# Kernel optimization log

Hardware: AMD Instinct MI355X
Metric: run time of the kernel (lower is better)

Reference implementation:

```python
import jax, jax.numpy as jnp
import numpy as np
import math

B, S, H = 2, 2048, 2048
NH, LD = 16, 512
HD = H // NH


def setup_inputs() -> dict:
    key = jax.random.key(0)
    ks = jax.random.split(key, 9)
    sc = 0.02
    return {
        "x": jax.random.normal(ks[0], (B, S, H), dtype=jnp.float32),
        "wq": jax.random.normal(ks[1], (H, H), dtype=jnp.float32) * sc,
        "bq": jnp.zeros((H,), dtype=jnp.float32),
        "wk_lat": jax.random.normal(ks[2], (H, LD), dtype=jnp.float32) * sc,
        "wv_lat": jax.random.normal(ks[3], (H, LD), dtype=jnp.float32) * sc,
        "wk": jax.random.normal(ks[4], (LD, H), dtype=jnp.float32) * sc,
        "wv": jax.random.normal(ks[5], (LD, H), dtype=jnp.float32) * sc,
        "wo": jax.random.normal(ks[6], (H, H), dtype=jnp.float32) * sc,
        "bo": jnp.zeros((H,), dtype=jnp.float32),
    }


def reference(x, wq, bq, wk_lat, wv_lat, wk, wv, wo, bo):
    b, s, _ = x.shape
    # projections
    q = (x @ wq + bq).reshape(b, s, NH, HD).transpose(0, 2, 1, 3)  # [B,NH,S,HD]
    k_lat = x @ wk_lat  # [B,S,LD]
    v_lat = x @ wv_lat
    k = (k_lat @ wk).reshape(b, s, NH, HD).transpose(0, 2, 1, 3)
    v = (v_lat @ wv).reshape(b, s, NH, HD).transpose(0, 2, 1, 3)
    # causal attention
    scores = jnp.einsum('bhqd,bhkd->bhqk', q, k) / math.sqrt(HD)
    mask = jnp.tril(jnp.ones((s, s), dtype=bool))  # True = keep
    scores = jnp.where(mask, scores, -jnp.inf)
    weights = jax.nn.softmax(scores, axis=-1)
    out = jnp.einsum('bhqk,bhkd->bhqd', weights, v)
    out = out.transpose(0, 2, 1, 3).reshape(b, s, H)
    return out @ wo + bo
```

## Files before the change

### kernel.cpp

```cpp
#include <hip/hip_runtime.h>
#include <hip/hip_bf16.h>

#define PB   2
#define PS   2048
#define PH   2048
#define PNH  16
#define PLD  512
#define PHD  128
#define PM   (PB * PS)
#define PNCAT 3072
#define ATT_SCALE 0.08838834764831845f
#define ATT_MOFF 4.0f

typedef __attribute__((ext_vector_type(8))) short bf16x8;
typedef __attribute__((ext_vector_type(4))) float f32x4;

__device__ __forceinline__ float bf2f(unsigned int h) {
    return __uint_as_float(h << 16);
}
__device__ __forceinline__ unsigned short f2bf(float f) {
    unsigned int u = __float_as_uint(f);
    u += 0x7FFFu + ((u >> 16) & 1u);
    return (unsigned short)(u >> 16);
}

__device__ __forceinline__ void gl_lds16(const unsigned short* g, unsigned short* l) {
    __builtin_amdgcn_global_load_lds(
        (const __attribute__((address_space(1))) unsigned int*)g,
        (__attribute__((address_space(3))) unsigned int*)l, 16, 0, 0);
}

__global__ __launch_bounds__(256) void cast_f32_bf16_kernel(
    const float* __restrict__ in, unsigned short* __restrict__ out, int n)
{
    int i = (blockIdx.x * 256 + threadIdx.x) * 4;
    if (i >= n) return;
    float4 f = *(const float4*)(in + i);
    unsigned int a = (unsigned int)f2bf(f.x) | ((unsigned int)f2bf(f.y) << 16);
    unsigned int b = (unsigned int)f2bf(f.z) | ((unsigned int)f2bf(f.w) << 16);
    *(uint2*)(out + i) = make_uint2(a, b);
}

__global__ __launch_bounds__(256) void transpose_cast_kernel(
    const float* __restrict__ in, unsigned short* __restrict__ out, int R, int C)
{
    __shared__ float tile[32][33];
    int tx = threadIdx.x, ty = threadIdx.y;
    int r0 = blockIdx.y * 32, c0 = blockIdx.x * 32;
#pragma unroll
    for (int i = 0; i < 32; i += 8)
        tile[ty + i][tx] = in[(size_t)(r0 + ty + i) * C + (c0 + tx)];
    __syncthreads();
#pragma unroll
    for (int i = 0; i < 32; i += 8)
        out[(size_t)(c0 + ty + i) * R + (r0 + tx)] = f2bf(tile[tx][ty + i]);
}

template<int EPI, bool HAS_BIAS>
__global__ __launch_bounds__(256) void gemm128_kernel(
    const unsigned short* __restrict__ A, int lda,
    const unsigned short* __restrict__ BT,
    const float* __restrict__ bias, int nbias,
    void* __restrict__ Cout, int ldc,
    int M, int N, int K)
{
    __shared__ __align__(16) unsigned short As[128 * 32];
    __shared__ __align__(16) unsigned short Bs[128 * 32];

    const int tid  = threadIdx.x;
    const int wave = tid >> 6;
    const int lane = tid & 63;
    const int wm = wave >> 1, wn = wave & 1;
    const int quad = lane >> 4, l15 = lane & 15;
    const int bm = blockIdx.y * 128, bn = blockIdx.x * 128;

    f32x4 acc[4][4] = {};

    const int srow = wave * 32 + (lane >> 2);
    const int scol = (lane & 3) * 8;
    const unsigned short* aG = A  + (size_t)(bm + srow) * lda + scol;
    const unsigned short* bG = BT + (size_t)(bn + srow) * K + scol;
    unsigned short* aL = &As[wave * 32 * 32];
    unsigned short* bL = &Bs[wave * 32 * 32];

    for (int k0 = 0; k0 < K; k0 += 32) {
        gl_lds16(aG + k0,                    aL);
        gl_lds16(aG + k0 + (size_t)16 * lda, aL + 16 * 32);
        gl_lds16(bG + k0,                    bL);
        gl_lds16(bG + k0 + (size_t)16 * K,   bL + 16 * 32);
        __syncthreads();
        bf16x8 af[4], bfr[4];
#pragma unroll
        for (int i = 0; i < 4; ++i) {
            af[i]  = *(const bf16x8*)&As[(wm * 64 + i * 16 + l15) * 32 + quad * 8];
            bfr[i] = *(const bf16x8*)&Bs[(wn * 64 + i * 16 + l15) * 32 + quad * 8];
        }
#pragma unroll
        for (int i = 0; i < 4; ++i)
#pragma unroll
            for (int j = 0; j < 4; ++j)
                acc[i][j] = __builtin_amdgcn_mfma_f32_16x16x32_bf16(af[i], bfr[j], acc[i][j], 0, 0, 0);
        __syncthreads();
    }

#pragma unroll
    for (int i = 0; i < 4; ++i)
#pragma unroll
        for (int j = 0; j < 4; ++j)
#pragma unroll
            for (int r = 0; r < 4; ++r) {
                int row = bm + wm * 64 + i * 16 + quad * 4 + r;
                int col = bn + wn * 64 + j * 16 + l15;
                float val = acc[i][j][r];
                if (HAS_BIAS && col < nbias) val += bias[col];
                if (EPI == 2) {
                    int bb = row >> 11, s = row & 2047, hh = col >> 7, d = col & 127;
                    size_t idx = ((size_t)((bb << 4) + hh) << 18) + ((size_t)(s >> 6) << 13)
                               + ((d >> 3) << 9) + ((s & 63) << 3) + (d & 7);
                    ((unsigned short*)Cout)[idx] = f2bf(val);
                } else if (EPI == 3) {
                    int bb = row >> 11, s = row & 2047, hh = col >> 7, d = col & 127;
                    size_t idx = ((size_t)((bb << 4) + hh) << 18) + ((size_t)(s >> 6) << 13)
                               + (((s >> 3) & 7) << 10) + (d << 3) + (s & 7);
                    ((unsigned short*)Cout)[idx] = f2bf(val);
                } else if (EPI == 1) {
                    ((float*)Cout)[(size_t)row * ldc + col] = val;
                } else {
                    ((unsigned short*)Cout)[(size_t)row * ldc + col] = f2bf(val);
                }
            }
}

__global__ __launch_bounds__(256) void flash_attn_mfma_kernel(
    const unsigned short* __restrict__ q,
    const unsigned short* __restrict__ kswz,
    const unsigned short* __restrict__ vswz,
    unsigned short* __restrict__ o)
{
    __shared__ __align__(16) unsigned short Kl[2][8192];
    __shared__ __align__(16) unsigned short Vl[8192];
    __shared__ __align__(16) unsigned short Ps[4][16][72];

    const int tid  = threadIdx.x;
    const int wave = tid >> 6;
    const int lane = tid & 63;
    const int quad = lane >> 4, l15 = lane & 15;

    const int bid = blockIdx.x;
    const int qt = 31 - (bid >> 5);
    const int bh = bid & 31;
    const int b  = bh >> 4, h = bh & 15;
    const int q0 = qt * 64;

    const unsigned short* qbase = q + (size_t)(b * PS + q0) * PNCAT + h * PHD;
    const unsigned short* kbase = kswz + ((size_t)bh << 18);
    const unsigned short* vbase = vswz + ((size_t)bh << 18);

    auto stageK = [&](int it, int buf) {
        const unsigned short* kt = kbase + ((size_t)it << 13);
#pragma unroll
        for (int j = 0; j < 4; ++j)
            gl_lds16(kt + (wave * 4 + j) * 512 + lane * 8, &Kl[buf][(wave * 4 + j) * 512]);
    };
    auto stageV = [&](int it) {
        const unsigned short* vt = vbase + ((size_t)it << 13);
#pragma unroll
        for (int j = 0; j < 4; ++j)
            gl_lds16(vt + (wave * 4 + j) * 512 + lane * 8, &Vl[(wave * 4 + j) * 512]);
    };

    bf16x8 aq[4];
#pragma unroll
    for (int kk = 0; kk < 4; ++kk)
        aq[kk] = *(const bf16x8*)(qbase + (size_t)(wave * 16 + l15) * PNCAT + kk * 32 + quad * 8);

    bf16x8 vones;
#pragma unroll
    for (int j = 0; j < 8; ++j) vones[j] = (short)0x3F80;

    f32x4 oacc[8] = {};
    f32x4 lacc = {};

    stageK(0, 0);

    for (int it = 0; it <= qt; ++it) {
        const int cur = it & 1;
        __syncthreads();
        stageV(it);
        if (it < qt) stageK(it + 1, cur ^ 1);

        f32x4 sacc[4] = {};
#pragma unroll
        for (int kk = 0; kk < 4; ++kk)
#pragma unroll
            for (int n = 0; n < 4; ++n) {
                bf16x8 bk = *(const bf16x8*)&Kl[cur][((kk * 4 + quad) * 64 + n * 16 + l15) * 8];
                sacc[n] = __builtin_amdgcn_mfma_f32_16x16x32_bf16(aq[kk], bk, sacc[n], 0, 0, 0);
            }

        const bool diag = (it == qt);
#pragma unroll
        for (int n = 0; n < 4; ++n)
#pragma unroll
            for (int r = 0; r < 4; ++r) {
                float p = __expf(fmaf(sacc[n][r], ATT_SCALE, -ATT_MOFF));
                if (diag && (n * 16 + l15 > wave * 16 + quad * 4 + r)) p = 0.0f;
                Ps[wave][quad * 4 + r][n * 16 + l15] = f2bf(p);
            }

        __syncthreads();

#pragma unroll
        for (int kk = 0; kk < 2; ++kk) {
            bf16x8 ap = *(const bf16x8*)&Ps[wave][l15][kk * 32 + quad * 8];
            lacc = __builtin_amdgcn_mfma_f32_16x16x32_bf16(ap, vones, lacc, 0, 0, 0);
#pragma unroll
            for (int n = 0; n < 8; ++n) {
                bf16x8 bv = *(const bf16x8*)&Vl[((kk * 4 + quad) * 128 + n * 16 + l15) * 8];
                oacc[n] = __builtin_amdgcn_mfma_f32_16x16x32_bf16(ap, bv, oacc[n], 0, 0, 0);
            }
        }
    }

    float inv[4];
#pragma unroll
    for (int r = 0; r < 4; ++r) inv[r] = 1.0f / lacc[r];
#pragma unroll
    for (int n = 0; n < 8; ++n)
#pragma unroll
        for (int r = 0; r < 4; ++r) {
            int row = q0 + wave * 16 + quad * 4 + r;
            int col = h * PHD + n * 16 + l15;
            o[(size_t)(b * PS + row) * PH + col] = f2bf(oacc[n][r] * inv[r]);
        }
}

extern "C" void kernel_launch(void* const* d_in, const int* in_sizes, int n_in,
                              void* d_out, int out_size, void* d_ws, size_t ws_size,
                              hipStream_t stream)
{
    const float* x      = (const float*)d_in[0];
    const float* wq     = (const float*)d_in[1];
    const float* bq     = (const float*)d_in[2];
    const float* wk_lat = (const float*)d_in[3];
    const float* wv_lat = (const float*)d_in[4];
    const float* wk     = (const float*)d_in[5];
    const float* wv     = (const float*)d_in[6];
    const float* wo     = (const float*)d_in[7];
    const float* bo     = (const float*)d_in[8];
    float* out = (float*)d_out;

    char* ws = (char*)d_ws;
    size_t off = 0;
    auto alloc = [&](size_t bytes) -> void* {
        void* p = ws + off;
        off += (bytes + 255) & ~(size_t)255;
        return p;
    };
    unsigned short* xb    = (unsigned short*)alloc((size_t)PM * PH * 2);
    unsigned short* wcatT = (unsigned short*)alloc((size_t)PNCAT * PH * 2);
    unsigned short* wkT   = (unsigned short*)alloc((size_t)PH * PLD * 2);
    unsigned short* wvT   = (unsigned short*)alloc((size_t)PH * PLD * 2);
    unsigned short* woT   = (unsigned short*)alloc((size_t)PH * PH * 2);
    unsigned short* cat   = (unsigned short*)alloc((size_t)PM * PNCAT * 2);
    unsigned short* kswz  = (unsigned short*)alloc((size_t)PM * PH * 2);
    unsigned short* attn  = (unsigned short*)alloc((size_t)PM * PH * 2);
    unsigned short* vswz  = xb;

    unsigned short* wqT    = wcatT;
    unsigned short* wkLatT = wcatT + (size_t)PH * PH;
    unsigned short* wvLatT = wcatT + (size_t)(PH + PLD) * PH;

    dim3 tb(32, 8);

    cast_f32_bf16_kernel<<<(PM * PH) / 4 / 256, 256, 0, stream>>>(x, xb, PM * PH);
    transpose_cast_kernel<<<dim3(PH / 32,  PH / 32),  tb, 0, stream>>>(wq,     wqT,    PH,  PH);
    transpose_cast_kernel<<<dim3(PLD / 32, PH / 32),  tb, 0, stream>>>(wk_lat, wkLatT, PH,  PLD);
    transpose_cast_kernel<<<dim3(PLD / 32, PH / 32),  tb, 0, stream>>>(wv_lat, wvLatT, PH,  PLD);
    transpose_cast_kernel<<<dim3(PH / 32,  PLD / 32), tb, 0, stream>>>(wk,     wkT,    PLD, PH);
    transpose_cast_kernel<<<dim3(PH / 32,  PLD / 32), tb, 0, stream>>>(wv,     wvT,    PLD, PH);
    transpose_cast_kernel<<<dim3(PH / 32,  PH / 32),  tb, 0, stream>>>(wo,     woT,    PH,  PH);

    gemm128_kernel<0, true><<<dim3(PNCAT / 128, PM / 128), 256, 0, stream>>>(
        xb, PH, wcatT, bq, PH, cat, PNCAT, PM, PNCAT, PH);

    gemm128_kernel<2, false><<<dim3(PH / 128, PM / 128), 256, 0, stream>>>(
        cat + PH, PNCAT, wkT, nullptr, 0, kswz, 0, PM, PH, PLD);
    gemm128_kernel<3, false><<<dim3(PH / 128, PM / 128), 256, 0, stream>>>(
        cat + PH + PLD, PNCAT, wvT, nullptr, 0, vswz, 0, PM, PH, PLD);

    flash_attn_mfma_kernel<<<PB * PNH * (PS / 64), 256, 0, stream>>>(cat, kswz, vswz, attn);

    gemm128_kernel<1, true><<<dim3(PH / 128, PM / 128), 256, 0, stream>>>(
        attn, PH, woT, bo, PH, out, PH, PM, PH, PH);
}
```

Measured before the change: 381.9 us.

## Replace 128x128 GEMM with 8-wave double-buffered swizzled 256-wide pipelined GEMM

Swaps the simple single-buffered 128x128 bf16 MFMA GEMM for an 8-wave kernel with 256-wide (BM x 256) tiles, K-step 64, and double-buffered LDS filled by direct global-to-LDS loads interleaved across four compute phases. The LDS layout is XOR-swizzled to avoid bank conflicts, and workgroups are remapped across XCDs for L2 locality. s_setprio and explicit waitcnt/barriers are used to overlap loads with MFMA. The goal is to hide memory latency and raise MFMA utilization in the projection GEMMs, at the cost of more LDS per block, more registers and more complex synchronization.

```diff
diff --git a/kernel.cpp b/kernel.cpp
--- a/kernel.cpp
+++ b/kernel.cpp
@@ -15,9 +15,6 @@
 typedef __attribute__((ext_vector_type(8))) short bf16x8;
 typedef __attribute__((ext_vector_type(4))) float f32x4;
 
-__device__ __forceinline__ float bf2f(unsigned int h) {
-    return __uint_as_float(h << 16);
-}
 __device__ __forceinline__ unsigned short f2bf(float f) {
     unsigned int u = __float_as_uint(f);
     u += 0x7FFFu + ((u >> 16) & 1u);
@@ -29,6 +26,10 @@
         (const __attribute__((address_space(1))) unsigned int*)g,
         (__attribute__((address_space(3))) unsigned int*)l, 16, 0, 0);
 }
+
+#define VMCNT(n)   asm volatile("s_waitcnt vmcnt(" #n ")" ::: "memory")
+#define LGKM0()    asm volatile("s_waitcnt lgkmcnt(0)" ::: "memory")
+#define MEMFENCE() asm volatile("" ::: "memory")
 
 __global__ __launch_bounds__(256) void cast_f32_bf16_kernel(
     const float* __restrict__ in, unsigned short* __restrict__ out, int n)
@@ -56,62 +57,171 @@
         out[(size_t)(c0 + ty + i) * R + (r0 + tx)] = f2bf(tile[tx][ty + i]);
 }
 
-template<int EPI, bool HAS_BIAS>
-__global__ __launch_bounds__(256) void gemm128_kernel(
+template<int BM, int EPI, bool HAS_BIAS>
+__global__ __launch_bounds__(512, 2) void gemm8p_kernel(
     const unsigned short* __restrict__ A, int lda,
     const unsigned short* __restrict__ BT,
     const float* __restrict__ bias, int nbias,
-    void* __restrict__ Cout, int ldc,
-    int M, int N, int K)
+    void* __restrict__ Cout, int ldc, int K)
 {
-    __shared__ __align__(16) unsigned short As[128 * 32];
-    __shared__ __align__(16) unsigned short Bs[128 * 32];
+    constexpr int AH  = BM / 128;
+    constexpr int MR  = BM / 32;
+    constexpr int MH  = MR / 2;
+    constexpr int ASZ = BM * 64;
+    __shared__ __align__(16) unsigned short lds[2 * ASZ + 32768];
 
     const int tid  = threadIdx.x;
-    const int wave = tid >> 6;
-    const int lane = tid & 63;
-    const int wm = wave >> 1, wn = wave & 1;
+    const int wave = tid >> 6, lane = tid & 63;
+    const int wm = wave >> 2, wn = wave & 3;
     const int quad = lane >> 4, l15 = lane & 15;
-    const int bm = blockIdx.y * 128, bn = blockIdx.x * 128;
-
-    f32x4 acc[4][4] = {};
-
-    const int srow = wave * 32 + (lane >> 2);
-    const int scol = (lane & 3) * 8;
-    const unsigned short* aG = A  + (size_t)(bm + srow) * lda + scol;
-    const unsigned short* bG = BT + (size_t)(bn + srow) * K + scol;
-    unsigned short* aL = &As[wave * 32 * 32];
-    unsigned short* bL = &Bs[wave * 32 * 32];
-
-    for (int k0 = 0; k0 < K; k0 += 32) {
-        gl_lds16(aG + k0,                    aL);
-        gl_lds16(aG + k0 + (size_t)16 * lda, aL + 16 * 32);
-        gl_lds16(bG + k0,                    bL);
-        gl_lds16(bG + k0 + (size_t)16 * K,   bL + 16 * 32);
-        __syncthreads();
-        bf16x8 af[4], bfr[4];
-#pragma unroll
-        for (int i = 0; i < 4; ++i) {
-            af[i]  = *(const bf16x8*)&As[(wm * 64 + i * 16 + l15) * 32 + quad * 8];
-            bfr[i] = *(const bf16x8*)&Bs[(wn * 64 + i * 16 + l15) * 32 + quad * 8];
-        }
-#pragma unroll
-        for (int i = 0; i < 4; ++i)
-#pragma unroll
-            for (int j = 0; j < 4; ++j)
-                acc[i][j] = __builtin_amdgcn_mfma_f32_16x16x32_bf16(af[i], bfr[j], acc[i][j], 0, 0, 0);
-        __syncthreads();
+    const int sw = l15 & 7;
+
+    const int gx  = gridDim.x;
+    const int nwg = gx * gridDim.y;
+    int wg = blockIdx.y * gx + blockIdx.x;
+    if (!(nwg & 7)) wg = (wg & 7) * (nwg >> 3) + (wg >> 3);
+    const int bm = (wg / gx) * BM, bn = (wg % gx) * 256;
+
+    const int nt = K >> 6;
+
+    const int srow = tid >> 3;
+    const int scol = ((tid & 7) ^ (srow & 7)) << 3;
+    const unsigned short* Ag = A  + (size_t)(bm + srow) * lda + scol;
+    const unsigned short* Bg = BT + (size_t)(bn + srow) * K   + scol;
+    unsigned short* const ldsA = &lds[wave * 512];
+    unsigned short* const ldsB = &lds[2 * ASZ + wave * 512];
+
+    auto stA = [&](int kt, int h, int b) {
+        const unsigned short* g = Ag + (size_t)(h * 128) * lda + kt * 64;
+        unsigned short* l = ldsA + b * ASZ + h * 8192;
+        gl_lds16(g, l);
+        gl_lds16(g + (size_t)64 * lda, l + 4096);
+    };
+    auto stB = [&](int kt, int h, int b) {
+        const unsigned short* g = Bg + (size_t)(h * 128) * K + kt * 64;
+        unsigned short* l = ldsB + b * 16384 + h * 8192;
+        gl_lds16(g, l);
+        gl_lds16(g + (size_t)64 * K, l + 4096);
+    };
+
+    auto ldA = [&](int b, int m, int ks) -> bf16x8 {
+        int ra = wm * (BM / 2) + m * 16 + l15;
+        return *(const bf16x8*)&lds[b * ASZ + (ra >> 7) * 8192 + (ra & 127) * 64
+                                    + (((ks * 4 + quad) ^ sw) << 3)];
+    };
+    auto ldB = [&](int b, int j, int ks) -> bf16x8 {
+        int rb = wn * 64 + j * 16 + l15;
+        return *(const bf16x8*)&lds[2 * ASZ + b * 16384 + (rb >> 7) * 8192 + (rb & 127) * 64
+                                    + (((ks * 4 + quad) ^ sw) << 3)];
+    };
+
+    f32x4 acc[MR][4] = {};
+    bf16x8 af[MH][2], bl[2][2], bh[2][2];
+
+    stA(0, 0, 0);
+    if constexpr (AH == 2) stA(0, 1, 0);
+    stB(0, 0, 0);
+    stB(0, 1, 0);
+    if (nt > 1) { stA(1, 0, 1); VMCNT(2); } else { VMCNT(0); }
+    __builtin_amdgcn_s_barrier();
+    MEMFENCE();
+
+    for (int t = 0; t < nt; ++t) {
+        const int b = t & 1, nb = b ^ 1;
+        const bool s1 = (t + 1 < nt), s2 = (t + 2 < nt);
+
+#pragma unroll
+        for (int m = 0; m < MH; ++m)
+#pragma unroll
+            for (int ks = 0; ks < 2; ++ks) af[m][ks] = ldA(b, m, ks);
+#pragma unroll
+        for (int j = 0; j < 2; ++j)
+#pragma unroll
+            for (int ks = 0; ks < 2; ++ks) bl[j][ks] = ldB(b, j, ks);
+        if (s1) { if constexpr (AH == 2) stA(t + 1, 1, nb); else stB(t + 1, 0, nb); }
+        __builtin_amdgcn_s_barrier();
+        LGKM0();
+        __builtin_amdgcn_sched_barrier(0);
+        __builtin_amdgcn_s_setprio(1);
+#pragma unroll
+        for (int m = 0; m < MH; ++m)
+#pragma unroll
+            for (int j = 0; j < 2; ++j)
+#pragma unroll
+                for (int ks = 0; ks < 2; ++ks)
+                    acc[m][j] = __builtin_amdgcn_mfma_f32_16x16x32_bf16(af[m][ks], bl[j][ks], acc[m][j], 0, 0, 0);
+        __builtin_amdgcn_s_setprio(0);
+        __builtin_amdgcn_s_barrier();
+
+#pragma unroll
+        for (int j = 0; j < 2; ++j)
+#pragma unroll
+            for (int ks = 0; ks < 2; ++ks) bh[j][ks] = ldB(b, 2 + j, ks);
+        if (s1) stB(t + 1, 1, nb);
+        __builtin_amdgcn_s_barrier();
+        LGKM0();
+        __builtin_amdgcn_sched_barrier(0);
+        __builtin_amdgcn_s_setprio(1);
+#pragma unroll
+        for (int m = 0; m < MH; ++m)
+#pragma unroll
+            for (int j = 0; j < 2; ++j)
+#pragma unroll
+                for (int ks = 0; ks < 2; ++ks)
+                    acc[m][2 + j] = __builtin_amdgcn_mfma_f32_16x16x32_bf16(af[m][ks], bh[j][ks], acc[m][2 + j], 0, 0, 0);
+        __builtin_amdgcn_s_setprio(0);
+        __builtin_amdgcn_s_barrier();
+
+#pragma unroll
+        for (int m = 0; m < MH; ++m)
+#pragma unroll
+            for (int ks = 0; ks < 2; ++ks) af[m][ks] = ldA(b, MH + m, ks);
+        if (s1) { if constexpr (AH == 2) stB(t + 1, 0, nb); }
+        __builtin_amdgcn_s_barrier();
+        LGKM0();
+        __builtin_amdgcn_sched_barrier(0);
+        __builtin_amdgcn_s_setprio(1);
+#pragma unroll
+        for (int m = 0; m < MH; ++m)
+#pragma unroll
+            for (int j = 0; j < 2; ++j)
+#pragma unroll
+                for (int ks = 0; ks < 2; ++ks)
+                    acc[MH + m][2 + j] = __builtin_amdgcn_mfma_f32_16x16x32_bf16(af[m][ks], bh[j][ks], acc[MH + m][2 + j], 0, 0, 0);
+        __builtin_amdgcn_s_setprio(0);
+        __builtin_amdgcn_s_barrier();
+
+#pragma unroll
+        for (int j = 0; j < 2; ++j)
+#pragma unroll
+            for (int ks = 0; ks < 2; ++ks) bl[j][ks] = ldB(b, j, ks);
+        if (s2) stA(t + 2, 0, b);
+        __builtin_amdgcn_s_barrier();
+        LGKM0();
+        __builtin_amdgcn_sched_barrier(0);
+        __builtin_amdgcn_s_setprio(1);
+#pragma unroll
+        for (int m = 0; m < MH; ++m)
+#pragma unroll
+            for (int j = 0; j < 2; ++j)
+#pragma unroll
+                for (int ks = 0; ks < 2; ++ks)
+                    acc[MH + m][j] = __builtin_amdgcn_mfma_f32_16x16x32_bf16(af[m][ks], bl[j][ks], acc[MH + m][j], 0, 0, 0);
+        __builtin_amdgcn_s_setprio(0);
+        if (s2) { VMCNT(2); } else { VMCNT(0); }
+        __builtin_amdgcn_s_barrier();
+        MEMFENCE();
     }
 
 #pragma unroll
-    for (int i = 0; i < 4; ++i)
+    for (int m = 0; m < MR; ++m)
 #pragma unroll
         for (int j = 0; j < 4; ++j)
 #pragma unroll
             for (int r = 0; r < 4; ++r) {
-                int row = bm + wm * 64 + i * 16 + quad * 4 + r;
+                int row = bm + wm * (BM / 2) + m * 16 + quad * 4 + r;
                 int col = bn + wn * 64 + j * 16 + l15;
-                float val = acc[i][j][r];
+                float val = acc[m][j][r];
                 if (HAS_BIAS && col < nbias) val += bias[col];
                 if (EPI == 2) {
                     int bb = row >> 11, s = row & 2047, hh = col >> 7, d = col & 127;
@@ -281,16 +391,16 @@
     transpose_cast_kernel<<<dim3(PH / 32,  PLD / 32), tb, 0, stream>>>(wv,     wvT,    PLD, PH);
     transpose_cast_kernel<<<dim3(PH / 32,  PH / 32),  tb, 0, stream>>>(wo,     woT,    PH,  PH);
 
-    gemm128_kernel<0, true><<<dim3(PNCAT / 128, PM / 128), 256, 0, stream>>>(
-        xb, PH, wcatT, bq, PH, cat, PNCAT, PM, PNCAT, PH);
-
-    gemm128_kernel<2, false><<<dim3(PH / 128, PM / 128), 256, 0, stream>>>(
-        cat + PH, PNCAT, wkT, nullptr, 0, kswz, 0, PM, PH, PLD);
-    gemm128_kernel<3, false><<<dim3(PH / 128, PM / 128), 256, 0, stream>>>(
-        cat + PH + PLD, PNCAT, wvT, nullptr, 0, vswz, 0, PM, PH, PLD);
+    gemm8p_kernel<256, 0, true><<<dim3(PNCAT / 256, PM / 256), 512, 0, stream>>>(
+        xb, PH, wcatT, bq, PH, cat, PNCAT, PH);
+
+    gemm8p_kernel<128, 2, false><<<dim3(PH / 256, PM / 128), 512, 0, stream>>>(
+        cat + PH, PNCAT, wkT, nullptr, 0, kswz, 0, PLD);
+    gemm8p_kernel<128, 3, false><<<dim3(PH / 256, PM / 128), 512, 0, stream>>>(
+        cat + PH + PLD, PNCAT, wvT, nullptr, 0, vswz, 0, PLD);
 
     flash_attn_mfma_kernel<<<PB * PNH * (PS / 64), 256, 0, stream>>>(cat, kswz, vswz, attn);
 
-    gemm128_kernel<1, true><<<dim3(PH / 128, PM / 128), 256, 0, stream>>>(
-        attn, PH, woT, bo, PH, out, PH, PM, PH, PH);
-}
+    gemm8p_kernel<128, 1, true><<<dim3(PH / 256, PM / 128), 512, 0, stream>>>(
+        attn, PH, woT, bo, PH, out, PH, PH);
+}
```

After: 352.9 us. 1.08x faster.

## Rework GEMM with 64-wide K tiles, XOR-swizzled LDS, and XCD-aware block remap

Applied to the files above, without the earlier changes.

The GEMM kernel now stages 128x64 K-tiles instead of 128x32, which halves the number of barrier pairs per K loop. It XOR-swizzles the LDS column layout to avoid bank conflicts on the bf16x8 fragment reads. Workgroup IDs are remapped in groups of 8, apparently to spread neighbouring tiles across the chip's dies for L2 locality, and launch bounds request 3 blocks per CU. LDS per block doubles and there is still no double buffering, so occupancy and latency hiding depend on the register and LDS budget.

```diff
diff --git a/kernel.cpp b/kernel.cpp
--- a/kernel.cpp
+++ b/kernel.cpp
@@ -15,9 +15,6 @@
 typedef __attribute__((ext_vector_type(8))) short bf16x8;
 typedef __attribute__((ext_vector_type(4))) float f32x4;
 
-__device__ __forceinline__ float bf2f(unsigned int h) {
-    return __uint_as_float(h << 16);
-}
 __device__ __forceinline__ unsigned short f2bf(float f) {
     unsigned int u = __float_as_uint(f);
     u += 0x7FFFu + ((u >> 16) & 1u);
@@ -29,6 +26,8 @@
         (const __attribute__((address_space(1))) unsigned int*)g,
         (__attribute__((address_space(3))) unsigned int*)l, 16, 0, 0);
 }
+
+#define VMCNT(n)     asm volatile("s_waitcnt vmcnt(" #n ")" ::: "memory")
 
 __global__ __launch_bounds__(256) void cast_f32_bf16_kernel(
     const float* __restrict__ in, unsigned short* __restrict__ out, int n)
@@ -57,61 +56,83 @@
 }
 
 template<int EPI, bool HAS_BIAS>
-__global__ __launch_bounds__(256) void gemm128_kernel(
+__global__ __launch_bounds__(256, 3) void gemm97_kernel(
     const unsigned short* __restrict__ A, int lda,
     const unsigned short* __restrict__ BT,
     const float* __restrict__ bias, int nbias,
-    void* __restrict__ Cout, int ldc,
-    int M, int N, int K)
-{
-    __shared__ __align__(16) unsigned short As[128 * 32];
-    __shared__ __align__(16) unsigned short Bs[128 * 32];
+    void* __restrict__ Cout, int ldc, int K)
+{
+    __shared__ __align__(16) unsigned short As[128 * 64];
+    __shared__ __align__(16) unsigned short Bs[128 * 64];
 
     const int tid  = threadIdx.x;
-    const int wave = tid >> 6;
-    const int lane = tid & 63;
+    const int wave = tid >> 6, lane = tid & 63;
     const int wm = wave >> 1, wn = wave & 1;
     const int quad = lane >> 4, l15 = lane & 15;
-    const int bm = blockIdx.y * 128, bn = blockIdx.x * 128;
+    const int sw = l15 & 7;
+
+    const int gx  = gridDim.x;
+    const int nwg = gx * gridDim.y;
+    int wg = blockIdx.y * gx + blockIdx.x;
+    if (!(nwg & 7)) wg = (wg & 7) * (nwg >> 3) + (wg >> 3);
+    const int bm = (wg / gx) * 128, bn = (wg % gx) * 128;
+
+    const int nt = K >> 6;
+
+    const int srow = tid >> 3;
+    const int scol = ((tid & 7) ^ (srow & 7)) << 3;
+    const unsigned short* Ag = A  + (size_t)(bm + srow) * lda + scol;
+    const unsigned short* Bg = BT + (size_t)(bn + srow) * K   + scol;
+    unsigned short* const ldsA = &As[wave * 512];
+    unsigned short* const ldsB = &Bs[wave * 512];
+
+    auto ldA = [&](int m, int ks) -> bf16x8 {
+        int ra = wm * 64 + m * 16 + l15;
+        return *(const bf16x8*)&As[ra * 64 + (((ks * 4 + quad) ^ sw) << 3)];
+    };
+    auto ldB = [&](int j, int ks) -> bf16x8 {
+        int rb = wn * 64 + j * 16 + l15;
+        return *(const bf16x8*)&Bs[rb * 64 + (((ks * 4 + quad) ^ sw) << 3)];
+    };
 
     f32x4 acc[4][4] = {};
 
-    const int srow = wave * 32 + (lane >> 2);
-    const int scol = (lane & 3) * 8;
-    const unsigned short* aG = A  + (size_t)(bm + srow) * lda + scol;
-    const unsigned short* bG = BT + (size_t)(bn + srow) * K + scol;
-    unsigned short* aL = &As[wave * 32 * 32];
-    unsigned short* bL = &Bs[wave * 32 * 32];
-
-    for (int k0 = 0; k0 < K; k0 += 32) {
-        gl_lds16(aG + k0,                    aL);
-        gl_lds16(aG + k0 + (size_t)16 * lda, aL + 16 * 32);
-        gl_lds16(bG + k0,                    bL);
-        gl_lds16(bG + k0 + (size_t)16 * K,   bL + 16 * 32);
+    for (int kt = 0; kt < nt; ++kt) {
+        const int k0 = kt * 64;
+#pragma unroll
+        for (int s = 0; s < 4; ++s) {
+            gl_lds16(Ag + (size_t)(s * 32) * lda + k0, ldsA + s * 2048);
+            gl_lds16(Bg + (size_t)(s * 32) * K   + k0, ldsB + s * 2048);
+        }
+        VMCNT(0);
         __syncthreads();
-        bf16x8 af[4], bfr[4];
-#pragma unroll
-        for (int i = 0; i < 4; ++i) {
-            af[i]  = *(const bf16x8*)&As[(wm * 64 + i * 16 + l15) * 32 + quad * 8];
-            bfr[i] = *(const bf16x8*)&Bs[(wn * 64 + i * 16 + l15) * 32 + quad * 8];
+
+        bf16x8 bfr[4][2];
+#pragma unroll
+        for (int j = 0; j < 4; ++j)
+#pragma unroll
+            for (int ks = 0; ks < 2; ++ks) bfr[j][ks] = ldB(j, ks);
+#pragma unroll
+        for (int m = 0; m < 4; ++m) {
+            bf16x8 a0 = ldA(m, 0), a1 = ldA(m, 1);
+#pragma unroll
+            for (int j = 0; j < 4; ++j) {
+                acc[m][j] = __builtin_amdgcn_mfma_f32_16x16x32_bf16(a0, bfr[j][0], acc[m][j], 0, 0, 0);
+                acc[m][j] = __builtin_amdgcn_mfma_f32_16x16x32_bf16(a1, bfr[j][1], acc[m][j], 0, 0, 0);
+            }
         }
-#pragma unroll
-        for (int i = 0; i < 4; ++i)
-#pragma unroll
-            for (int j = 0; j < 4; ++j)
-                acc[i][j] = __builtin_amdgcn_mfma_f32_16x16x32_bf16(af[i], bfr[j], acc[i][j], 0, 0, 0);
         __syncthreads();
     }
 
 #pragma unroll
-    for (int i = 0; i < 4; ++i)
+    for (int m = 0; m < 4; ++m)
 #pragma unroll
         for (int j = 0; j < 4; ++j)
 #pragma unroll
             for (int r = 0; r < 4; ++r) {
-                int row = bm + wm * 64 + i * 16 + quad * 4 + r;
+                int row = bm + wm * 64 + m * 16 + quad * 4 + r;
                 int col = bn + wn * 64 + j * 16 + l15;
-                float val = acc[i][j][r];
+                float val = acc[m][j][r];
                 if (HAS_BIAS && col < nbias) val += bias[col];
                 if (EPI == 2) {
                     int bb = row >> 11, s = row & 2047, hh = col >> 7, d = col & 127;
@@ -281,16 +302,16 @@
     transpose_cast_kernel<<<dim3(PH / 32,  PLD / 32), tb, 0, stream>>>(wv,     wvT,    PLD, PH);
     transpose_cast_kernel<<<dim3(PH / 32,  PH / 32),  tb, 0, stream>>>(wo,     woT,    PH,  PH);
 
-    gemm128_kernel<0, true><<<dim3(PNCAT / 128, PM / 128), 256, 0, stream>>>(
-        xb, PH, wcatT, bq, PH, cat, PNCAT, PM, PNCAT, PH);
-
-    gemm128_kernel<2, false><<<dim3(PH / 128, PM / 128), 256, 0, stream>>>(
-        cat + PH, PNCAT, wkT, nullptr, 0, kswz, 0, PM, PH, PLD);
-    gemm128_kernel<3, false><<<dim3(PH / 128, PM / 128), 256, 0, stream>>>(
-        cat + PH + PLD, PNCAT, wvT, nullptr, 0, vswz, 0, PM, PH, PLD);
+    gemm97_kernel<0, true><<<dim3(PNCAT / 128, PM / 128), 256, 0, stream>>>(
+        xb, PH, wcatT, bq, PH, cat, PNCAT, PH);
+
+    gemm97_kernel<2, false><<<dim3(PH / 128, PM / 128), 256, 0, stream>>>(
+        cat + PH, PNCAT, wkT, nullptr, 0, kswz, 0, PLD);
+    gemm97_kernel<3, false><<<dim3(PH / 128, PM / 128), 256, 0, stream>>>(
+        cat + PH + PLD, PNCAT, wvT, nullptr, 0, vswz, 0, PLD);
 
     flash_attn_mfma_kernel<<<PB * PNH * (PS / 64), 256, 0, stream>>>(cat, kswz, vswz, attn);
 
-    gemm128_kernel<1, true><<<dim3(PH / 128, PM / 128), 256, 0, stream>>>(
-        attn, PH, woT, bo, PH, out, PH, PM, PH, PH);
-}
+    gemm97_kernel<1, true><<<dim3(PH / 128, PM / 128), 256, 0, stream>>>(
+        attn, PH, woT, bo, PH, out, PH, PH);
+}
```

Result: faster. 343.5 us (-10.0%).
